# Kernel tuning notes

Measured on AMD Instinct MI355X. Metric: run time of the kernel, lower is better.

Reference implementation:

```python
import jax, jax.numpy as jnp
import numpy as np

B, LQ, LK = 4, 2048, 2048
DQ, DC = 1024, 1024
H, DH = 16, 64
INNER = H * DH
LN_EPS = 1e-5
TAU_INIT = DH ** -0.5


def layernorm(x, w, b):
    mu = jnp.mean(x, axis=-1, keepdims=True)
    var = jnp.var(x, axis=-1, keepdims=True)
    return (x - mu) * jax.lax.rsqrt(var + LN_EPS) * w + b


def l2norm(x, eps=1e-12):
    # matches F.normalize(dim=-1): x / max(||x||, eps)
    n = jnp.sqrt(jnp.sum(x * x, axis=-1, keepdims=True))
    return x / jnp.maximum(n, eps)


def setup_inputs() -> dict:
    key = jax.random.key(0)
    ks = jax.random.split(key, 8)
    s = lambda d: (1.0 / np.sqrt(d)).astype(np.float32) if isinstance(d, np.ndarray) else np.float32(1.0 / np.sqrt(d))
    return {
        "x": jax.random.normal(ks[0], (B, LQ, DQ), jnp.float32),
        "context": jax.random.normal(ks[1], (B, LK, DC), jnp.float32),
        "key_padding_mask": jax.random.bernoulli(ks[2], 0.1, (B, LK)),
        "ln_q_w": jnp.ones((DQ,), jnp.float32),
        "ln_q_b": jnp.zeros((DQ,), jnp.float32),
        "ln_ctx_w": jnp.ones((DC,), jnp.float32),
        "ln_ctx_b": jnp.zeros((DC,), jnp.float32),
        "Wq": jax.random.normal(ks[3], (DQ, INNER), jnp.float32) * s(DQ),
        "Wk": jax.random.normal(ks[4], (DC, INNER), jnp.float32) * s(DC),
        "Wv": jax.random.normal(ks[5], (DC, INNER), jnp.float32) * s(DC),
        "Wo": jax.random.normal(ks[6], (INNER, DQ), jnp.float32) * s(INNER),
        "tau": jnp.float32(TAU_INIT),
    }


def reference(x, context, key_padding_mask, ln_q_w, ln_q_b, ln_ctx_w, ln_ctx_b, Wq, Wk, Wv, Wo, tau):
    q_in = layernorm(x, ln_q_w, ln_q_b)
    kv_in = layernorm(context, ln_ctx_w, ln_ctx_b)
    q = (q_in @ Wq).reshape(B, LQ, H, DH)   # [B,Lq,H,Dh]
    k = (kv_in @ Wk).reshape(B, LK, H, DH)
    v = (kv_in @ Wv).reshape(B, LK, H, DH)
    q = l2norm(q)
    k = l2norm(k)
    scores = jnp.einsum('bqhd,bkhd->bhqk', q, k) / (tau + 1e-6)
    scores = jnp.where(key_padding_mask[:, None, None, :], -jnp.inf, scores)
    attn = jax.nn.softmax(scores, axis=-1)
    out = jnp.einsum('bhqk,bkhd->bqhd', attn, v).reshape(B, LQ, INNER)
    return out @ Wo
```

## Files before the change

kernel.cpp:

```cpp
#include <hip/hip_runtime.h>

typedef unsigned short u16;
typedef __bf16 bf16x8 __attribute__((ext_vector_type(8)));
typedef short s16x4 __attribute__((ext_vector_type(4)));
typedef float f32x4 __attribute__((ext_vector_type(4)));

__device__ __forceinline__ u16 f2bf(float f) {
  unsigned u = __float_as_uint(f);
  unsigned r = u + 0x7fffu + ((u >> 16) & 1u);
  return (u16)(r >> 16);
}

__device__ __forceinline__ unsigned cvt_pk(float a, float b) {
  unsigned r;
  asm("v_cvt_pk_bf16_f32 %0, %1, %2" : "=v"(r) : "v"(a), "v"(b));
  return r;
}

#if __has_builtin(__builtin_amdgcn_exp2f)
#define EXP2(x) __builtin_amdgcn_exp2f(x)
#else
#define EXP2(x) exp2f(x)
#endif

__device__ __forceinline__ void async_cp16(const void* g, void* l) {
  __builtin_amdgcn_global_load_lds((__attribute__((address_space(1))) void*)g,
                                   (__attribute__((address_space(3))) void*)l,
                                   16, 0, 0);
}

#define MFMA32(a, b, c) __builtin_amdgcn_mfma_f32_16x16x32_bf16(a, b, c, 0, 0, 0)

#if __has_builtin(__builtin_amdgcn_mfma_f32_16x16x16bf16_1k)
#define MFMA16(a, b, c) __builtin_amdgcn_mfma_f32_16x16x16bf16_1k(a, b, c, 0, 0, 0)
#else
__device__ __forceinline__ f32x4 mfma16_fb(s16x4 a, s16x4 b, f32x4 c) {
  asm("v_mfma_f32_16x16x16_bf16 %0, %1, %2, %0" : "+v"(c) : "v"(a), "v"(b));
  return c;
}
#define MFMA16(a, b, c) mfma16_fb(a, b, c)
#endif

__global__ __launch_bounds__(256)
void ln_cast2(const float* __restrict__ X0, const float* __restrict__ X1,
              const float* __restrict__ W0, const float* __restrict__ B0,
              const float* __restrict__ W1, const float* __restrict__ B1,
              u16* __restrict__ Y0, u16* __restrict__ Y1) {
  __shared__ float red[8];
  const int blk = blockIdx.x, t = threadIdx.x;
  const int sel = blk >> 13;
  const int row = blk & 8191;
  const float* X = sel ? X1 : X0;
  const float* W = sel ? W1 : W0;
  const float* Bv = sel ? B1 : B0;
  u16* Y = sel ? Y1 : Y0;
  const int wave = t >> 6, lane = t & 63;
  const float4 v = ((const float4*)(X + (size_t)row * 1024))[t];
  float s  = v.x + v.y + v.z + v.w;
  float ss = v.x*v.x + v.y*v.y + v.z*v.z + v.w*v.w;
#pragma unroll
  for (int m = 32; m; m >>= 1) { s += __shfl_xor(s, m, 64); ss += __shfl_xor(ss, m, 64); }
  if (lane == 0) { red[wave] = s; red[4 + wave] = ss; }
  __syncthreads();
  float S  = red[0] + red[1] + red[2] + red[3];
  float SS = red[4] + red[5] + red[6] + red[7];
  float mu  = S * (1.0f / 1024.0f);
  float var = SS * (1.0f / 1024.0f) - mu * mu;
  float rstd = rsqrtf(var + 1e-5f);
  const float4 wv = ((const float4*)W)[t];
  const float4 bv = ((const float4*)Bv)[t];
  ushort4 o;
  o.x = f2bf((v.x - mu) * rstd * wv.x + bv.x);
  o.y = f2bf((v.y - mu) * rstd * wv.y + bv.y);
  o.z = f2bf((v.z - mu) * rstd * wv.z + bv.z);
  o.w = f2bf((v.w - mu) * rstd * wv.w + bv.w);
  ((ushort4*)(Y + (size_t)row * 1024))[t] = o;
}

__global__ __launch_bounds__(256)
void wtrans4(const float* __restrict__ Wq, const float* __restrict__ Wk,
             const float* __restrict__ Wv, const float* __restrict__ Wo,
             u16* __restrict__ WqT, u16* __restrict__ WkT,
             u16* __restrict__ WvT, u16* __restrict__ WoT) {
  __shared__ float t[64][65];
  const int z = blockIdx.z;
  const float* W = z == 0 ? Wq : (z == 1 ? Wk : (z == 2 ? Wv : Wo));
  u16* WT = z == 0 ? WqT : (z == 1 ? WkT : (z == 2 ? WvT : WoT));
  const int k0 = blockIdx.y * 64, n0 = blockIdx.x * 64;
  const int lr = threadIdx.x >> 4, lc = threadIdx.x & 15;
#pragma unroll
  for (int r = 0; r < 4; ++r) {
    int row = r * 16 + lr;
    float4 v = *(const float4*)(W + (size_t)(k0 + row) * 1024 + n0 + lc * 4);
    t[row][lc*4+0] = v.x; t[row][lc*4+1] = v.y; t[row][lc*4+2] = v.z; t[row][lc*4+3] = v.w;
  }
  __syncthreads();
#pragma unroll
  for (int r = 0; r < 4; ++r) {
    int n = r * 16 + lr;
    ushort4 o;
    o.x = f2bf(t[lc*4+0][n]); o.y = f2bf(t[lc*4+1][n]);
    o.z = f2bf(t[lc*4+2][n]); o.w = f2bf(t[lc*4+3][n]);
    *(ushort4*)(WT + (size_t)(n0 + n) * 1024 + k0 + lc * 4) = o;
  }
}

__global__ __launch_bounds__(256)
void vtrans(const float* __restrict__ V, u16* __restrict__ VT) {
  __shared__ float t[64][65];
  const int b = blockIdx.z, h = blockIdx.y, kk0 = blockIdx.x * 64;
  const int lr = threadIdx.x >> 4, lc = threadIdx.x & 15;
#pragma unroll
  for (int r = 0; r < 4; ++r) {
    int row = r * 16 + lr;
    float4 v = *(const float4*)(V + (size_t)(b * 2048 + kk0 + row) * 1024 + h * 64 + lc * 4);
    t[row][lc*4+0] = v.x; t[row][lc*4+1] = v.y; t[row][lc*4+2] = v.z; t[row][lc*4+3] = v.w;
  }
  __syncthreads();
#pragma unroll
  for (int r = 0; r < 4; ++r) {
    int d = r * 16 + lr;
    ushort4 o;
    o.x = f2bf(t[lc*4+0][d]); o.y = f2bf(t[lc*4+1][d]);
    o.z = f2bf(t[lc*4+2][d]); o.w = f2bf(t[lc*4+3][d]);
    *(ushort4*)(VT + ((size_t)(b * 16 + h) * 64 + d) * 2048 + kk0 + lc * 4) = o;
  }
}

__global__ __launch_bounds__(256, 2)
void gemm_qkv(const u16* __restrict__ qin, const u16* __restrict__ kvin,
              const u16* __restrict__ WqT, const u16* __restrict__ WkT,
              const u16* __restrict__ WvT,
              u16* __restrict__ qbf, u16* __restrict__ kbf,
              float* __restrict__ vscr, const float* __restrict__ taup) {
  __shared__ __align__(16) u16 As[128 * 64];
  __shared__ __align__(16) u16 Bs[128 * 64];
  const int z = blockIdx.z;
  const u16* A  = z == 0 ? qin : kvin;
  const u16* Bt = z == 0 ? WqT : (z == 1 ? WkT : WvT);
  const int tid = threadIdx.x;
  const int wave = tid >> 6, lane = tid & 63;
  const int quad = lane >> 4, l15 = lane & 15;
  const int m0 = blockIdx.y * 128, n0 = blockIdx.x * 128;
  const int wm = (wave >> 1) * 64, wn = (wave & 1) * 64;
  const int srow = lane >> 3, scol = (lane & 7) * 8;
  const int K = 1024, N = 1024;

  const f32x4 fz = {0.f, 0.f, 0.f, 0.f};
  f32x4 acc[4][4];
#pragma unroll
  for (int i = 0; i < 4; ++i)
#pragma unroll
    for (int j = 0; j < 4; ++j) acc[i][j] = fz;

  for (int kt = 0; kt < K; kt += 64) {
    __syncthreads();
#pragma unroll
    for (int r = 0; r < 4; ++r) {
      const int c = r * 4 + wave;
      const int row = c * 8 + srow;
      async_cp16(A  + (size_t)(m0 + row) * K + kt + scol, (char*)As + c * 1024);
      async_cp16(Bt + (size_t)(n0 + row) * K + kt + scol, (char*)Bs + c * 1024);
    }
    __syncthreads();
#pragma unroll
    for (int ks = 0; ks < 2; ++ks) {
      bf16x8 af[4], bfr[4];
#pragma unroll
      for (int i = 0; i < 4; ++i)
        af[i] = *(const bf16x8*)(const void*)(As + (wm + i * 16 + l15) * 64 + ks * 32 + quad * 8);
#pragma unroll
      for (int j = 0; j < 4; ++j)
        bfr[j] = *(const bf16x8*)(const void*)(Bs + (wn + j * 16 + l15) * 64 + ks * 32 + quad * 8);
#pragma unroll
      for (int i = 0; i < 4; ++i)
#pragma unroll
        for (int j = 0; j < 4; ++j)
          acc[i][j] = MFMA32(af[i], bfr[j], acc[i][j]);
    }
  }

  if (z < 2) {
    const float tsc = z == 0 ? 1.44269504f / (taup[0] + 1e-6f) : 1.0f;
    u16* Y = z == 0 ? qbf : kbf;
#pragma unroll
    for (int i = 0; i < 4; ++i)
#pragma unroll
      for (int e = 0; e < 4; ++e) {
        float ss = 0.f;
#pragma unroll
        for (int j = 0; j < 4; ++j) ss = fmaf(acc[i][j][e], acc[i][j][e], ss);
        ss += __shfl_xor(ss, 1, 64); ss += __shfl_xor(ss, 2, 64);
        ss += __shfl_xor(ss, 4, 64); ss += __shfl_xor(ss, 8, 64);
        float sc = tsc / fmaxf(sqrtf(ss), 1e-12f);
        int row = m0 + wm + i * 16 + quad * 4 + e;
#pragma unroll
        for (int j = 0; j < 4; ++j)
          Y[(size_t)row * N + n0 + wn + j * 16 + l15] = f2bf(acc[i][j][e] * sc);
      }
  } else {
#pragma unroll
    for (int i = 0; i < 4; ++i)
#pragma unroll
      for (int j = 0; j < 4; ++j)
#pragma unroll
        for (int e = 0; e < 4; ++e) {
          int row = m0 + wm + i * 16 + quad * 4 + e;
          int col = n0 + wn + j * 16 + l15;
          vscr[(size_t)row * N + col] = acc[i][j][e];
        }
  }
}

__global__ __launch_bounds__(256, 2)
void gemm_bt(const u16* __restrict__ A, const u16* __restrict__ Bt,
             float* __restrict__ C, int M, int N, int K) {
  __shared__ __align__(16) u16 As[128 * 64];
  __shared__ __align__(16) u16 Bs[128 * 64];
  const int tid = threadIdx.x;
  const int wave = tid >> 6, lane = tid & 63;
  const int quad = lane >> 4, l15 = lane & 15;
  const int m0 = blockIdx.y * 128, n0 = blockIdx.x * 128;
  const int wm = (wave >> 1) * 64, wn = (wave & 1) * 64;
  const int srow = lane >> 3, scol = (lane & 7) * 8;

  const f32x4 fz = {0.f, 0.f, 0.f, 0.f};
  f32x4 acc[4][4];
#pragma unroll
  for (int i = 0; i < 4; ++i)
#pragma unroll
    for (int j = 0; j < 4; ++j) acc[i][j] = fz;

  for (int kt = 0; kt < K; kt += 64) {
    __syncthreads();
#pragma unroll
    for (int r = 0; r < 4; ++r) {
      const int c = r * 4 + wave;
      const int row = c * 8 + srow;
      async_cp16(A  + (size_t)(m0 + row) * K + kt + scol, (char*)As + c * 1024);
      async_cp16(Bt + (size_t)(n0 + row) * K + kt + scol, (char*)Bs + c * 1024);
    }
    __syncthreads();
#pragma unroll
    for (int ks = 0; ks < 2; ++ks) {
      bf16x8 af[4], bfr[4];
#pragma unroll
      for (int i = 0; i < 4; ++i)
        af[i] = *(const bf16x8*)(const void*)(As + (wm + i * 16 + l15) * 64 + ks * 32 + quad * 8);
#pragma unroll
      for (int j = 0; j < 4; ++j)
        bfr[j] = *(const bf16x8*)(const void*)(Bs + (wn + j * 16 + l15) * 64 + ks * 32 + quad * 8);
#pragma unroll
      for (int i = 0; i < 4; ++i)
#pragma unroll
        for (int j = 0; j < 4; ++j)
          acc[i][j] = MFMA32(af[i], bfr[j], acc[i][j]);
    }
  }
#pragma unroll
  for (int i = 0; i < 4; ++i)
#pragma unroll
    for (int j = 0; j < 4; ++j)
#pragma unroll
      for (int e = 0; e < 4; ++e) {
        int row = m0 + wm + i * 16 + quad * 4 + e;
        int col = n0 + wn + j * 16 + l15;
        C[(size_t)row * N + col] = acc[i][j][e];
      }
}

__global__ __launch_bounds__(256, 2)
void flash_attn10(const u16* __restrict__ Qb, const u16* __restrict__ Kb,
                  const u16* __restrict__ Vt, const int* __restrict__ mask,
                  u16* __restrict__ Ob) {
  __shared__ __align__(16) u16 SH[16384];
  __shared__ __align__(16) float Msf[2048];
  const int tid = threadIdx.x, w = tid >> 6, lane = tid & 63;
  const int quad = lane >> 4, l15 = lane & 15;
  const int b = blockIdx.z, h = blockIdx.y, q0 = blockIdx.x * 128;
  const int srow = lane >> 3;
  const int scolX = ((lane & 7) ^ srow) * 8;
  const int fsw = ((l15 & 7) << 4);

#pragma unroll
  for (int r = 0; r < 4; ++r) {
    int c = w * 4 + r;
    async_cp16(Qb + (size_t)(b * 2048 + q0 + c * 8 + srow) * 1024 + h * 64 + scolX,
               (char*)SH + c * 1024);
  }
  {
    const int* mp = mask + b * 2048 + tid * 8;
    int4 ma = *(const int4*)mp;
    int4 mb = *(const int4*)(mp + 4);
    float4 o0, o1;
    o0.x = ma.x ? -3.0e38f : 0.f; o0.y = ma.y ? -3.0e38f : 0.f;
    o0.z = ma.z ? -3.0e38f : 0.f; o0.w = ma.w ? -3.0e38f : 0.f;
    o1.x = mb.x ? -3.0e38f : 0.f; o1.y = mb.y ? -3.0e38f : 0.f;
    o1.z = mb.z ? -3.0e38f : 0.f; o1.w = mb.w ? -3.0e38f : 0.f;
    *(float4*)(Msf + tid * 8)     = o0;
    *(float4*)(Msf + tid * 8 + 4) = o1;
  }
  __syncthreads();

  bf16x8 aq[2][2];
#pragma unroll
  for (int i = 0; i < 2; ++i)
#pragma unroll
    for (int ks = 0; ks < 2; ++ks)
      aq[i][ks] = *(const bf16x8*)(const void*)(
          (const char*)SH + (w * 32 + i * 16 + l15) * 128 + (((ks * 4 + quad) << 4) ^ fsw));
  __syncthreads();

#pragma unroll
  for (int r = 0; r < 2; ++r) {
    int c = w * 2 + r;
    async_cp16(Kb + (size_t)(b * 2048 + c * 8 + srow) * 1024 + h * 64 + scolX,
               (char*)SH + c * 1024);
    async_cp16(Vt + ((size_t)(b * 16 + h) * 64 + c * 8 + srow) * 2048 + scolX,
               (char*)SH + 16384 + c * 1024);
  }
  __syncthreads();

  const f32x4 fz = {0.f, 0.f, 0.f, 0.f};
  f32x4 o[4][2];
  float rs[2] = {0.f, 0.f};
#pragma unroll
  for (int dt = 0; dt < 4; ++dt)
#pragma unroll
    for (int i = 0; i < 2; ++i) o[dt][i] = fz;

  int cur = 0;
  for (int kt = 0; kt < 2048; kt += 64) {
    const char* Kc = (const char*)SH + cur * 8192;
    const char* Vc = (const char*)SH + 16384 + cur * 8192;
    if (kt + 64 < 2048) {
      char* Kn = (char*)SH + (cur ^ 1) * 8192;
      char* Vn = (char*)SH + 16384 + (cur ^ 1) * 8192;
#pragma unroll
      for (int r = 0; r < 2; ++r) {
        int c = w * 2 + r;
        async_cp16(Kb + (size_t)(b * 2048 + kt + 64 + c * 8 + srow) * 1024 + h * 64 + scolX,
                   Kn + c * 1024);
        async_cp16(Vt + ((size_t)(b * 16 + h) * 64 + c * 8 + srow) * 2048 + kt + 64 + scolX,
                   Vn + c * 1024);
      }
    }

    bf16x8 kb[4][2];
#pragma unroll
    for (int kkt = 0; kkt < 4; ++kkt)
#pragma unroll
      for (int ks = 0; ks < 2; ++ks)
        kb[kkt][ks] = *(const bf16x8*)(const void*)(
            Kc + (kkt * 16 + l15) * 128 + (((ks * 4 + quad) << 4) ^ fsw));

#pragma unroll
    for (int kkt = 0; kkt < 4; ++kkt) {
      f32x4 bias = *(const f32x4*)(Msf + kt + kkt * 16 + quad * 4);

      s16x4 pf[2];
#pragma unroll
      for (int i = 0; i < 2; ++i) {
        f32x4 st = MFMA32(kb[kkt][0], aq[i][0], bias);
        st = MFMA32(kb[kkt][1], aq[i][1], st);
        float p0 = EXP2(st[0]), p1 = EXP2(st[1]);
        float p2 = EXP2(st[2]), p3 = EXP2(st[3]);
        rs[i] += (p0 + p1) + (p2 + p3);
        union { unsigned u[2]; s16x4 s; } pk;
        pk.u[0] = cvt_pk(p0, p1);
        pk.u[1] = cvt_pk(p2, p3);
        pf[i] = pk.s;
      }
      __builtin_amdgcn_s_setprio(1);
#pragma unroll
      for (int dt = 0; dt < 4; ++dt) {
        s16x4 va = *(const s16x4*)(const void*)(
            Vc + (dt * 16 + l15) * 128 + ((kkt * 32 + quad * 8) ^ fsw));
#pragma unroll
        for (int i = 0; i < 2; ++i)
          o[dt][i] = MFMA16(va, pf[i], o[dt][i]);
      }
      __builtin_amdgcn_s_setprio(0);
    }
    __syncthreads();
    cur ^= 1;
  }

  float inv[2];
#pragma unroll
  for (int i = 0; i < 2; ++i) {
    float v = rs[i];
    v += __shfl_xor(v, 16, 64);
    v += __shfl_xor(v, 32, 64);
    inv[i] = 1.0f / v;
  }

  u16* strip = SH + w * 2048;
#pragma unroll
  for (int dt = 0; dt < 4; ++dt)
#pragma unroll
    for (int i = 0; i < 2; ++i) {
      union { unsigned u[2]; s16x4 s; } pk;
      pk.u[0] = cvt_pk(o[dt][i][0] * inv[i], o[dt][i][1] * inv[i]);
      pk.u[1] = cvt_pk(o[dt][i][2] * inv[i], o[dt][i][3] * inv[i]);
      *(s16x4*)(void*)((char*)strip + (i * 16 + l15) * 128 + ((dt * 32 + quad * 8) ^ fsw)) = pk.s;
    }
#pragma unroll
  for (int pass = 0; pass < 4; ++pass) {
    int row = pass * 8 + (lane >> 3), oct = lane & 7;
    int4 v = *(const int4*)(const void*)((const char*)strip + row * 128 + ((oct ^ (row & 7)) << 4));
    *(int4*)(Ob + (size_t)(b * 2048 + q0 + w * 32 + row) * 1024 + h * 64 + oct * 8) = v;
  }
}

extern "C" void kernel_launch(void* const* d_in, const int* in_sizes, int n_in,
                              void* d_out, int out_size, void* d_ws, size_t ws_size,
                              hipStream_t stream) {
  const float* x    = (const float*)d_in[0];
  const float* ctx  = (const float*)d_in[1];
  const int*   mask = (const int*)d_in[2];
  const float* lnqw = (const float*)d_in[3];
  const float* lnqb = (const float*)d_in[4];
  const float* lncw = (const float*)d_in[5];
  const float* lncb = (const float*)d_in[6];
  const float* Wq   = (const float*)d_in[7];
  const float* Wk   = (const float*)d_in[8];
  const float* Wv   = (const float*)d_in[9];
  const float* Wo   = (const float*)d_in[10];
  const float* tau  = (const float*)d_in[11];
  float* out = (float*)d_out;
  char* ws = (char*)d_ws;
  const size_t MB = 1024 * 1024;

  u16* qin  = (u16*)(ws + 0 * MB);
  u16* kvin = (u16*)(ws + 16 * MB);
  u16* WqT  = (u16*)(ws + 32 * MB);
  u16* WkT  = (u16*)(ws + 34 * MB);
  u16* WvT  = (u16*)(ws + 36 * MB);
  u16* WoT  = (u16*)(ws + 38 * MB);
  u16* qbf  = (u16*)(ws + 40 * MB);
  u16* kbf  = (u16*)(ws + 56 * MB);
  u16* vT   = (u16*)(ws + 72 * MB);
  float* scr = out;
  u16* attn = qin;

  ln_cast2<<<16384, 256, 0, stream>>>(x, ctx, lnqw, lnqb, lncw, lncb, qin, kvin);
  wtrans4<<<dim3(16, 16, 4), 256, 0, stream>>>(Wq, Wk, Wv, Wo, WqT, WkT, WvT, WoT);

  gemm_qkv<<<dim3(8, 64, 3), 256, 0, stream>>>(qin, kvin, WqT, WkT, WvT,
                                               qbf, kbf, scr, tau);

  vtrans<<<dim3(32, 16, 4), 256, 0, stream>>>(scr, vT);

  flash_attn10<<<dim3(16, 16, 4), 256, 0, stream>>>(qbf, kbf, vT, mask, attn);

  gemm_bt<<<dim3(8, 64), 256, 0, stream>>>(attn, WoT, out, 8192, 1024, 1024);
}
```

Baseline: 335.3 us.

## Fuse V transpose and bf16 cast into QKV GEMM epilogue

The V projection tile is now converted to bf16 in the GEMM epilogue, transposed through a swizzled shared-memory buffer, and written straight into the head-major V^T layout. This removes the separate vtrans kernel, along with the fp32 scratch write and re-read of V (32 MB each way). In exchange the V blocks do two extra barriers and a shared-memory pass, and the As/Bs buffers are merged into one 32 KB array that is reused for the transpose.

```diff
diff --git a/kernel.cpp b/kernel.cpp
--- a/kernel.cpp
+++ b/kernel.cpp
@@ -105,36 +105,15 @@
   }
 }
 
-__global__ __launch_bounds__(256)
-void vtrans(const float* __restrict__ V, u16* __restrict__ VT) {
-  __shared__ float t[64][65];
-  const int b = blockIdx.z, h = blockIdx.y, kk0 = blockIdx.x * 64;
-  const int lr = threadIdx.x >> 4, lc = threadIdx.x & 15;
-#pragma unroll
-  for (int r = 0; r < 4; ++r) {
-    int row = r * 16 + lr;
-    float4 v = *(const float4*)(V + (size_t)(b * 2048 + kk0 + row) * 1024 + h * 64 + lc * 4);
-    t[row][lc*4+0] = v.x; t[row][lc*4+1] = v.y; t[row][lc*4+2] = v.z; t[row][lc*4+3] = v.w;
-  }
-  __syncthreads();
-#pragma unroll
-  for (int r = 0; r < 4; ++r) {
-    int d = r * 16 + lr;
-    ushort4 o;
-    o.x = f2bf(t[lc*4+0][d]); o.y = f2bf(t[lc*4+1][d]);
-    o.z = f2bf(t[lc*4+2][d]); o.w = f2bf(t[lc*4+3][d]);
-    *(ushort4*)(VT + ((size_t)(b * 16 + h) * 64 + d) * 2048 + kk0 + lc * 4) = o;
-  }
-}
-
 __global__ __launch_bounds__(256, 2)
 void gemm_qkv(const u16* __restrict__ qin, const u16* __restrict__ kvin,
               const u16* __restrict__ WqT, const u16* __restrict__ WkT,
               const u16* __restrict__ WvT,
               u16* __restrict__ qbf, u16* __restrict__ kbf,
-              float* __restrict__ vscr, const float* __restrict__ taup) {
-  __shared__ __align__(16) u16 As[128 * 64];
-  __shared__ __align__(16) u16 Bs[128 * 64];
+              u16* __restrict__ vT, const float* __restrict__ taup) {
+  __shared__ __align__(16) u16 shbuf[128 * 128];
+  u16* As = shbuf;
+  u16* Bs = shbuf + 128 * 64;
   const int z = blockIdx.z;
   const u16* A  = z == 0 ? qin : kvin;
   const u16* Bt = z == 0 ? WqT : (z == 1 ? WkT : WvT);
@@ -199,16 +178,30 @@
           Y[(size_t)row * N + n0 + wn + j * 16 + l15] = f2bf(acc[i][j][e] * sc);
       }
   } else {
+    __syncthreads();
+    u16* T = shbuf;
 #pragma unroll
     for (int i = 0; i < 4; ++i)
 #pragma unroll
-      for (int j = 0; j < 4; ++j)
-#pragma unroll
-        for (int e = 0; e < 4; ++e) {
-          int row = m0 + wm + i * 16 + quad * 4 + e;
-          int col = n0 + wn + j * 16 + l15;
-          vscr[(size_t)row * N + col] = acc[i][j][e];
-        }
+      for (int j = 0; j < 4; ++j) {
+        int col = wn + j * 16 + l15;
+        int kkb = (wm + i * 16 + quad * 4) * 2;
+        union { unsigned u[2]; s16x4 s; } pk;
+        pk.u[0] = cvt_pk(acc[i][j][0], acc[i][j][1]);
+        pk.u[1] = cvt_pk(acc[i][j][2], acc[i][j][3]);
+        *(s16x4*)(void*)((char*)T + col * 256 + (kkb ^ ((col & 7) << 4))) = pk.s;
+      }
+    __syncthreads();
+    const int bb = m0 >> 11, kk0 = m0 & 2047;
+    const int col = tid >> 1, half = tid & 1;
+    const int hh = (n0 + col) >> 6, d = (n0 + col) & 63;
+    u16* dst = vT + ((size_t)(bb * 16 + hh) * 64 + d) * 2048 + kk0 + half * 64;
+#pragma unroll
+    for (int p = 0; p < 8; ++p) {
+      int kkb = (half * 64 + p * 8) * 2;
+      int4 v = *(const int4*)(const void*)((const char*)T + col * 256 + (kkb ^ ((col & 7) << 4)));
+      *(int4*)(dst + p * 8) = v;
+    }
   }
 }
 
@@ -441,16 +434,13 @@
   u16* qbf  = (u16*)(ws + 40 * MB);
   u16* kbf  = (u16*)(ws + 56 * MB);
   u16* vT   = (u16*)(ws + 72 * MB);
-  float* scr = out;
   u16* attn = qin;
 
   ln_cast2<<<16384, 256, 0, stream>>>(x, ctx, lnqw, lnqb, lncw, lncb, qin, kvin);
   wtrans4<<<dim3(16, 16, 4), 256, 0, stream>>>(Wq, Wk, Wv, Wo, WqT, WkT, WvT, WoT);
 
   gemm_qkv<<<dim3(8, 64, 3), 256, 0, stream>>>(qin, kvin, WqT, WkT, WvT,
-                                               qbf, kbf, scr, tau);
-
-  vtrans<<<dim3(32, 16, 4), 256, 0, stream>>>(scr, vT);
+                                               qbf, kbf, vT, tau);
 
   flash_attn10<<<dim3(16, 16, 4), 256, 0, stream>>>(qbf, kbf, vT, mask, attn);
 
```

Measured after the change: 337.0 us. Within noise of the previous version (+0.5%).
